# Performance work log

Hardware: AMD Instinct MI355X
Metric: run time of the kernel (lower is better)

The kernel has to match this reference:

```python
import jax, jax.numpy as jnp
import numpy as np

S = 7          # number of slots
B = 8192       # batch
D = 1024       # input_dim
E = 256        # slot_embedding_dim
H = 512        # rnn_hidden_dim
SH = 256       # slot_hidden_dim
V = 100        # labels per slot (uniform)


def _lstm_cell(x, h, c, W_ih, W_hh, b_ih, b_hh):
    # PyTorch LSTMCell: gates ordered i, f, g, o
    gates = x @ W_ih.T + b_ih + h @ W_hh.T + b_hh
    i, f, g, o = jnp.split(gates, 4, axis=-1)
    i = jax.nn.sigmoid(i); f = jax.nn.sigmoid(f)
    g = jnp.tanh(g); o = jax.nn.sigmoid(o)
    c_new = f * c + i * g
    h_new = o * jnp.tanh(c_new)
    return h_new, c_new


def setup_inputs() -> dict:
    key = jax.random.key(0)
    ks = jax.random.split(key, 24)
    sc = 0.05
    D0 = D + E  # layer-0 input size
    inp = {
        'inputs': jax.random.normal(ks[0], (B, D), jnp.float32),
        'labels': jax.random.randint(ks[1], (S - 1, B), 0, V),
        'start': jax.random.normal(ks[2], (E,), jnp.float32),
        'emb': jax.random.normal(ks[3], (S - 1, V, E), jnp.float32) * sc,
        # layer 0 (input size D0)
        'W_ih0': jax.random.normal(ks[4], (S, 4 * H, D0), jnp.float32) * sc,
        'W_hh0': jax.random.normal(ks[5], (S, 4 * H, H), jnp.float32) * sc,
        'b_ih0': jax.random.normal(ks[6], (S, 4 * H), jnp.float32) * sc,
        'b_hh0': jax.random.normal(ks[7], (S, 4 * H), jnp.float32) * sc,
        'hwN_W0': jax.random.normal(ks[8], (S, H, D0 + H), jnp.float32) * sc,
        'hwN_b0': jax.random.normal(ks[9], (S, H), jnp.float32) * sc,
        'hwL_W0': jax.random.normal(ks[10], (S, H, D0), jnp.float32) * sc,
        # layer 1 (input size H)
        'W_ih1': jax.random.normal(ks[11], (S, 4 * H, H), jnp.float32) * sc,
        'W_hh1': jax.random.normal(ks[12], (S, 4 * H, H), jnp.float32) * sc,
        'b_ih1': jax.random.normal(ks[13], (S, 4 * H), jnp.float32) * sc,
        'b_hh1': jax.random.normal(ks[14], (S, 4 * H), jnp.float32) * sc,
        'hwN_W1': jax.random.normal(ks[15], (S, H, H + H), jnp.float32) * sc,
        'hwN_b1': jax.random.normal(ks[16], (S, H), jnp.float32) * sc,
        'hwL_W1': jax.random.normal(ks[17], (S, H, H), jnp.float32) * sc,
        # slot hidden + classifier
        'sh_W': jax.random.normal(ks[18], (S, SH, H), jnp.float32) * sc,
        'sh_b': jax.random.normal(ks[19], (S, SH), jnp.float32) * sc,
        'pred_W': jax.random.normal(ks[20], (S, V, SH), jnp.float32) * sc,
        'pred_b': jax.random.normal(ks[21], (S, V), jnp.float32) * sc,
    }
    return inp


def reference(inputs, labels, start, emb,
              W_ih0, W_hh0, b_ih0, b_hh0, hwN_W0, hwN_b0, hwL_W0,
              W_ih1, W_hh1, b_ih1, b_hh1, hwN_W1, hwN_b1, hwL_W1,
              sh_W, sh_b, pred_W, pred_b):
    bsz = inputs.shape[0]
    cur_emb = jnp.broadcast_to(start[None, :], (bsz, E))
    h0 = jnp.zeros((bsz, H), inputs.dtype); c0 = jnp.zeros((bsz, H), inputs.dtype)
    h1 = jnp.zeros((bsz, H), inputs.dtype); c1 = jnp.zeros((bsz, H), inputs.dtype)
    logits_all = []
    for i in range(S):  # slots are a short, structurally distinct recurrence
        x = jnp.concatenate([inputs, cur_emb], axis=-1)  # [B, D+E]
        # layer 0
        h0, c0 = _lstm_cell(x, h0, c0, W_ih0[i], W_hh0[i], b_ih0[i], b_hh0[i])
        gate = jax.nn.sigmoid(jnp.concatenate([x, h0], -1) @ hwN_W0[i].T + hwN_b0[i])
        cur = gate * h0 + (1.0 - gate) * (x @ hwL_W0[i].T)
        # layer 1
        h1, c1 = _lstm_cell(cur, h1, c1, W_ih1[i], W_hh1[i], b_ih1[i], b_hh1[i])
        gate1 = jax.nn.sigmoid(jnp.concatenate([cur, h1], -1) @ hwN_W1[i].T + hwN_b1[i])
        # (highway output of last layer feeds nothing further for this slot)
        _ = gate1 * h1 + (1.0 - gate1) * (cur @ hwL_W1[i].T)
        hidden = jax.nn.relu(h1 @ sh_W[i].T + sh_b[i])     # [B, SH]
        logits_all.append(hidden @ pred_W[i].T + pred_b[i])  # [B, V]
        if i < S - 1:
            cur_emb = emb[i][labels[i]]  # teacher-forced embedding lookup
    return jnp.stack(logits_all, axis=0)  # [S, B, V]
```

## Files before the change

### kernel.cpp

```cpp
#include <hip/hip_runtime.h>

#define SLOTS 7
#define BATCH 8192

typedef __attribute__((ext_vector_type(8))) __bf16 bf16x8;
typedef __attribute__((ext_vector_type(4))) float f32x4;

__device__ __forceinline__ void gl_lds16(const __bf16* g, __bf16* l) {
  __builtin_amdgcn_global_load_lds(
      (const __attribute__((address_space(1))) void*)g,
      (__attribute__((address_space(3))) void*)l, 16, 0, 0);
}

__device__ __forceinline__ float sigmoidf_(float x) {
  return 1.f / (1.f + __expf(-x));
}
__device__ __forceinline__ float tanhf_(float x) {
  float xc = fminf(fmaxf(x, -15.f), 15.f);
  float e = __expf(2.f * xc);
  return (e - 1.f) / (e + 1.f);
}

__device__ __forceinline__ void xcd_remap(int& bx, int& by) {
  const int NBx = gridDim.x;
  const int NB = NBx * gridDim.y;
  int id = by * NBx + bx;
  id = (id & 7) * (NB >> 3) + (id >> 3);
  bx = id % NBx;
  by = id / NBx;
}

__global__ void __launch_bounds__(256, 4)
gemm_lstm(const __bf16* __restrict__ A, int lda,
          const __bf16* __restrict__ Bw, int ldb,
          const float* __restrict__ b_ih, const float* __restrict__ b_hh,
          float* __restrict__ cst, __bf16* __restrict__ hout, int hld, int hoff,
          int K) {
  __shared__ __align__(16) __bf16 As[2][128 * 32];
  __shared__ __align__(16) __bf16 Bs[2][128 * 32];
  const int w = threadIdx.x >> 6;
  const int lane = threadIdx.x & 63;
  const int wr = w >> 1, wc = w & 1;
  int bx = blockIdx.x, by = blockIdx.y;
  xcd_remap(bx, by);
  const int rowBase = by << 7;
  const int colBase = bx << 7;
  const int sr = lane >> 2;
  const int scs = (((lane & 3) ^ ((sr >> 1) & 3)) << 3);

  f32x4 acc[4][4];
#pragma unroll
  for (int i = 0; i < 4; ++i)
#pragma unroll
    for (int j = 0; j < 4; ++j) acc[i][j] = (f32x4){0.f, 0.f, 0.f, 0.f};

  const int nsteps = K >> 5;

#define STAGE(bi, k0)                                                            \
  {                                                                              \
    const __bf16* ga = A + (size_t)(rowBase + (w << 5) + sr) * lda + (k0) + scs; \
    gl_lds16(ga, &As[(bi)][(w << 5) * 32]);                                      \
    gl_lds16(ga + (size_t)16 * lda, &As[(bi)][((w << 5) + 16) * 32]);            \
    const __bf16* gb = Bw + (size_t)(colBase + (w << 5) + sr) * ldb + (k0) + scs;\
    gl_lds16(gb, &Bs[(bi)][(w << 5) * 32]);                                      \
    gl_lds16(gb + (size_t)16 * ldb, &Bs[(bi)][((w << 5) + 16) * 32]);            \
  }

  STAGE(0, 0);
  __syncthreads();
  int buf = 0;
  const int ln = lane & 15;
  const int lh = lane >> 4;
  const int swz = ((lh ^ ((ln >> 1) & 3)) << 3);
  for (int t = 0; t < nsteps; ++t) {
    if (t + 1 < nsteps) STAGE(buf ^ 1, (t + 1) << 5);
    bf16x8 av[4], bv[4];
#pragma unroll
    for (int i = 0; i < 4; ++i)
      av[i] = *(const bf16x8*)&As[buf][((wr << 6) + (i << 4) + ln) * 32 + swz];
#pragma unroll
    for (int i = 0; i < 4; ++i)
      bv[i] = *(const bf16x8*)&Bs[buf][((wc << 6) + (i << 4) + ln) * 32 + swz];
#pragma unroll
    for (int mi = 0; mi < 4; ++mi)
#pragma unroll
      for (int ni = 0; ni < 4; ++ni)
        acc[mi][ni] = __builtin_amdgcn_mfma_f32_16x16x32_bf16(
            av[mi], bv[ni], acc[mi][ni], 0, 0, 0);
    __syncthreads();
    buf ^= 1;
  }
#undef STAGE

  const int row0 = rowBase + (wr << 6) + (lh << 2);
  const int h = (((colBase >> 6) + wc) << 4) + ln;
  const float bs0 = b_ih[h] + b_hh[h];
  const float bs1 = b_ih[512 + h] + b_hh[512 + h];
  const float bs2 = b_ih[1024 + h] + b_hh[1024 + h];
  const float bs3 = b_ih[1536 + h] + b_hh[1536 + h];
#pragma unroll
  for (int mi = 0; mi < 4; ++mi)
#pragma unroll
    for (int r = 0; r < 4; ++r) {
      const int row = row0 + (mi << 4) + r;
      float gi = sigmoidf_(acc[mi][0][r] + bs0);
      float gf = sigmoidf_(acc[mi][1][r] + bs1);
      float gg = tanhf_(acc[mi][2][r] + bs2);
      float go = sigmoidf_(acc[mi][3][r] + bs3);
      const size_t ci = (size_t)row * 512 + h;
      float cn = gf * cst[ci] + gi * gg;
      cst[ci] = cn;
      hout[(size_t)row * hld + hoff + h] = (__bf16)(go * tanhf_(cn));
    }
}

template <int MODE>
__global__ void __launch_bounds__(256)
gemm_bt(const __bf16* __restrict__ A, int lda,
        const __bf16* __restrict__ Bw, int ldb,
        void* __restrict__ Cout, int ldc,
        const float* __restrict__ bias,
        const __bf16* __restrict__ auxr,
        __bf16* __restrict__ hout, int hld, int hoff,
        const __bf16* __restrict__ hsrc,
        const float* __restrict__ embp, const int* __restrict__ labels, int do_emb,
        int M, int N, int K, int Nreal) {
  __shared__ __align__(16) __bf16 As[2][128 * 32];
  __shared__ __align__(16) __bf16 Bs[2][128 * 32];
  const int w = threadIdx.x >> 6;
  const int lane = threadIdx.x & 63;
  const int wr = w >> 1, wc = w & 1;
  int bx = blockIdx.x, by = blockIdx.y;
  xcd_remap(bx, by);
  const int rowBase = by << 7;
  const int colBase = bx << 7;
  const int sr = lane >> 2;
  const int sc = (lane & 3) << 3;

  f32x4 acc[4][4];
#pragma unroll
  for (int i = 0; i < 4; ++i)
#pragma unroll
    for (int j = 0; j < 4; ++j) acc[i][j] = (f32x4){0.f, 0.f, 0.f, 0.f};

  const int nsteps = K >> 5;

#define STAGE(bi, k0)                                                           \
  {                                                                             \
    const __bf16* ga = A + (size_t)(rowBase + (w << 5) + sr) * lda + (k0) + sc; \
    gl_lds16(ga, &As[(bi)][(w << 5) * 32]);                                     \
    gl_lds16(ga + (size_t)16 * lda, &As[(bi)][((w << 5) + 16) * 32]);           \
    const __bf16* gb = Bw + (size_t)(colBase + (w << 5) + sr) * ldb + (k0) + sc;\
    gl_lds16(gb, &Bs[(bi)][(w << 5) * 32]);                                     \
    gl_lds16(gb + (size_t)16 * ldb, &Bs[(bi)][((w << 5) + 16) * 32]);           \
  }

  STAGE(0, 0);
  __syncthreads();
  int buf = 0;
  const int ln = lane & 15;
  const int kg = (lane >> 4) << 3;
  for (int t = 0; t < nsteps; ++t) {
    if (t + 1 < nsteps) STAGE(buf ^ 1, (t + 1) << 5);
    bf16x8 av[4], bv[4];
#pragma unroll
    for (int i = 0; i < 4; ++i)
      av[i] = *(const bf16x8*)&As[buf][((wr << 6) + (i << 4) + ln) * 32 + kg];
#pragma unroll
    for (int i = 0; i < 4; ++i)
      bv[i] = *(const bf16x8*)&Bs[buf][((wc << 6) + (i << 4) + ln) * 32 + kg];
#pragma unroll
    for (int mi = 0; mi < 4; ++mi)
#pragma unroll
      for (int ni = 0; ni < 4; ++ni)
        acc[mi][ni] = __builtin_amdgcn_mfma_f32_16x16x32_bf16(
            av[mi], bv[ni], acc[mi][ni], 0, 0, 0);
    __syncthreads();
    buf ^= 1;
  }
#undef STAGE

  const int lh = lane >> 4;
  const int row0 = rowBase + (wr << 6) + (lh << 2);
  const int col0 = colBase + (wc << 6) + ln;

  if (MODE == 1) {
    __bf16* C = (__bf16*)Cout;
#pragma unroll
    for (int mi = 0; mi < 4; ++mi)
#pragma unroll
      for (int ni = 0; ni < 4; ++ni) {
        const int col = col0 + (ni << 4);
        const float b = bias[col];
#pragma unroll
        for (int r = 0; r < 4; ++r) {
          float v = fmaxf(acc[mi][ni][r] + b, 0.f);
          C[(size_t)(row0 + (mi << 4) + r) * ldc + col] = (__bf16)v;
        }
      }
  } else if (MODE == 2) {
    float* C = (float*)Cout;
#pragma unroll
    for (int mi = 0; mi < 4; ++mi)
#pragma unroll
      for (int ni = 0; ni < 4; ++ni) {
        const int col = col0 + (ni << 4);
        if (col < Nreal) {
          const float b = bias[col];
#pragma unroll
          for (int r = 0; r < 4; ++r)
            C[(size_t)(row0 + (mi << 4) + r) * ldc + col] = acc[mi][ni][r] + b;
        }
      }
  } else if (MODE == 7) {
    __bf16* C = (__bf16*)Cout;
#pragma unroll
    for (int mi = 0; mi < 4; ++mi)
#pragma unroll
      for (int ni = 0; ni < 4; ++ni) {
        const int col = col0 + (ni << 4);
#pragma unroll
        for (int r = 0; r < 4; ++r)
          C[(size_t)(row0 + (mi << 4) + r) * ldc + col] = (__bf16)acc[mi][ni][r];
      }
  } else if (MODE == 6) {
    __bf16* C = (__bf16*)Cout;
#pragma unroll
    for (int mi = 0; mi < 4; ++mi)
#pragma unroll
      for (int ni = 0; ni < 4; ++ni) {
        const int col = col0 + (ni << 4);
#pragma unroll
        for (int r = 0; r < 4; ++r) {
          const int row = row0 + (mi << 4) + r;
          float xp = (float)auxr[(size_t)row * 1024 + col];
          float hwl = (float)auxr[(size_t)row * 1024 + 512 + col];
          float gn = sigmoidf_(acc[mi][ni][r] + xp + bias[col]);
          float hn = (float)hsrc[(size_t)row * 512 + col];
          C[(size_t)row * ldc + col] = (__bf16)(gn * hn + (1.f - gn) * hwl);
          hout[(size_t)row * hld + hoff + col] = (__bf16)hn;
        }
      }
    if (do_emb && colBase < 256) {
#pragma unroll
      for (int mi = 0; mi < 4; ++mi)
#pragma unroll
        for (int r = 0; r < 4; ++r) {
          const int row = row0 + (mi << 4) + r;
          const int lab = labels[row];
#pragma unroll
          for (int ni = 0; ni < 4; ++ni) {
            const int col = col0 + (ni << 4);
            hout[(size_t)row * hld + 1024 + col] =
                (__bf16)embp[(size_t)lab * 256 + col];
          }
        }
    }
  }
}

#define PR0 2621440
#define PR1 3670016
#define PR2 4325376
#define PR3 4980736
#define PR4 5242880
#define PR5 6291456
#define PR6 7340032
#define PR7 7471104
#define PR8 7503872
__global__ void pack_all(const float* __restrict__ W_ih0, const float* __restrict__ W_hh0,
                         const float* __restrict__ hwN_W0, const float* __restrict__ hwL_W0,
                         const float* __restrict__ W_ih1, const float* __restrict__ W_hh1,
                         const float* __restrict__ sh_W, const float* __restrict__ pred_W,
                         __bf16* __restrict__ WA, __bf16* __restrict__ WX,
                         __bf16* __restrict__ WH, __bf16* __restrict__ WB,
                         __bf16* __restrict__ WS, __bf16* __restrict__ WP, int s) {
  const int idx = blockIdx.x * 256 + threadIdx.x;
  if (idx >= PR8) return;
  if (idx < PR0) {
    int i = idx, r = i / 1280, c = i - r * 1280;
    int sr = (((r >> 4) & 3) << 9) + ((r >> 6) << 4) + (r & 15);
    WA[(long)r * 1792 + c] = (__bf16)W_ih0[(size_t)s * 2048 * 1280 + (long)sr * 1280 + c];
  } else if (idx < PR1) {
    int i = idx - PR0, r = i >> 9, c = i & 511;
    int sr = (((r >> 4) & 3) << 9) + ((r >> 6) << 4) + (r & 15);
    WA[(long)r * 1792 + 1280 + c] = (__bf16)W_hh0[(size_t)s * 2048 * 512 + (long)sr * 512 + c];
  } else if (idx < PR2) {
    int i = idx - PR1, r = i / 1280, c = i - r * 1280;
    WX[(long)r * 1280 + c] = (__bf16)hwN_W0[(size_t)s * 512 * 1792 + (long)r * 1792 + c];
  } else if (idx < PR3) {
    int i = idx - PR2, r = i / 1280, c = i - r * 1280;
    WX[(long)(512 + r) * 1280 + c] = (__bf16)hwL_W0[(size_t)s * 512 * 1280 + (long)r * 1280 + c];
  } else if (idx < PR4) {
    int i = idx - PR3, r = i >> 9, c = i & 511;
    WH[(long)r * 512 + c] = (__bf16)hwN_W0[(size_t)s * 512 * 1792 + (long)r * 1792 + 1280 + c];
  } else if (idx < PR5) {
    int i = idx - PR4, r = i >> 9, c = i & 511;
    int sr = (((r >> 4) & 3) << 9) + ((r >> 6) << 4) + (r & 15);
    WB[(long)r * 1024 + c] = (__bf16)W_ih1[(size_t)s * 2048 * 512 + (long)sr * 512 + c];
  } else if (idx < PR6) {
    int i = idx - PR5, r = i >> 9, c = i & 511;
    int sr = (((r >> 4) & 3) << 9) + ((r >> 6) << 4) + (r & 15);
    WB[(long)r * 1024 + 512 + c] = (__bf16)W_hh1[(size_t)s * 2048 * 512 + (long)sr * 512 + c];
  } else if (idx < PR7) {
    int i = idx - PR6, r = i >> 9, c = i & 511;
    WS[(long)r * 512 + c] = (__bf16)sh_W[(size_t)s * 256 * 512 + (long)r * 512 + c];
  } else {
    int i = idx - PR7, r = i >> 8, c = i & 255;
    float v = (r < 100) ? pred_W[(size_t)s * 100 * 256 + (long)r * 256 + c] : 0.f;
    WP[(long)r * 256 + c] = (__bf16)v;
  }
}

__global__ void conv_inputs(const float* __restrict__ in, __bf16* __restrict__ xh) {
  int idx = blockIdx.x * 256 + threadIdx.x;
  int b = idx >> 10, c = idx & 1023;
  xh[(size_t)b * 1792 + c] = (__bf16)in[idx];
}

__global__ void set_start(const float* __restrict__ start, __bf16* __restrict__ xh) {
  int idx = blockIdx.x * 256 + threadIdx.x;
  int b = idx >> 8, e = idx & 255;
  xh[(size_t)b * 1792 + 1024 + e] = (__bf16)start[e];
}

__global__ void zero_states(__bf16* __restrict__ xh, __bf16* __restrict__ xh1A) {
  int idx = blockIdx.x * 256 + threadIdx.x;
  int b = idx >> 9, h = idx & 511;
  xh[(size_t)b * 1792 + 1280 + h] = (__bf16)0.f;
  xh1A[(size_t)b * 1024 + 512 + h] = (__bf16)0.f;
}

extern "C" void kernel_launch(void* const* d_in, const int* in_sizes, int n_in,
                              void* d_out, int out_size, void* d_ws, size_t ws_size,
                              hipStream_t stream) {
  const float* inputs = (const float*)d_in[0];
  const int* labels = (const int*)d_in[1];
  const float* start = (const float*)d_in[2];
  const float* emb = (const float*)d_in[3];
  const float* W_ih0 = (const float*)d_in[4];
  const float* W_hh0 = (const float*)d_in[5];
  const float* b_ih0 = (const float*)d_in[6];
  const float* b_hh0 = (const float*)d_in[7];
  const float* hwN_W0 = (const float*)d_in[8];
  const float* hwN_b0 = (const float*)d_in[9];
  const float* hwL_W0 = (const float*)d_in[10];
  const float* W_ih1 = (const float*)d_in[11];
  const float* W_hh1 = (const float*)d_in[12];
  const float* b_ih1 = (const float*)d_in[13];
  const float* b_hh1 = (const float*)d_in[14];
  const float* sh_W = (const float*)d_in[18];
  const float* sh_b = (const float*)d_in[19];
  const float* pred_W = (const float*)d_in[20];
  const float* pred_b = (const float*)d_in[21];
  float* out = (float*)d_out;

  char* p = (char*)d_ws;
  size_t off = 0;
  auto alloc = [&](size_t bytes) {
    void* r = p + off;
    off += (bytes + 255) & ~(size_t)255;
    return r;
  };
  __bf16* WA = (__bf16*)alloc((size_t)2048 * 1792 * 2);
  __bf16* WX = (__bf16*)alloc((size_t)1024 * 1280 * 2);
  __bf16* WH = (__bf16*)alloc((size_t)512 * 512 * 2);
  __bf16* WB = (__bf16*)alloc((size_t)2048 * 1024 * 2);
  __bf16* WS = (__bf16*)alloc((size_t)256 * 512 * 2);
  __bf16* WP = (__bf16*)alloc((size_t)128 * 256 * 2);
  __bf16* xh = (__bf16*)alloc((size_t)BATCH * 1792 * 2);
  __bf16* xh1A = (__bf16*)alloc((size_t)BATCH * 1024 * 2);
  __bf16* xh1B = (__bf16*)alloc((size_t)BATCH * 1024 * 2);
  __bf16* h0new = (__bf16*)alloc((size_t)BATCH * 512 * 2);
  __bf16* ghw = (__bf16*)alloc((size_t)BATCH * 1024 * 2);
  float* c0 = (float*)alloc((size_t)BATCH * 512 * 4);
  float* c1 = (float*)alloc((size_t)BATCH * 512 * 4);
  __bf16* hidden = (__bf16*)ghw;
  (void)ws_size; (void)in_sizes; (void)n_in; (void)out_size;

  hipMemsetAsync(c0, 0, (size_t)BATCH * 512 * 4, stream);
  hipMemsetAsync(c1, 0, (size_t)BATCH * 512 * 4, stream);
  zero_states<<<BATCH * 512 / 256, 256, 0, stream>>>(xh, xh1A);
  conv_inputs<<<BATCH * 1024 / 256, 256, 0, stream>>>(inputs, xh);
  set_start<<<BATCH * 256 / 256, 256, 0, stream>>>(start, xh);

  const dim3 blk(256);
  for (int s = 0; s < SLOTS; ++s) {
    __bf16* xcur = (s & 1) ? xh1B : xh1A;
    __bf16* xnext = (s & 1) ? xh1A : xh1B;
    pack_all<<<(PR8 + 255) / 256, blk, 0, stream>>>(
        W_ih0, W_hh0, hwN_W0, hwL_W0, W_ih1, W_hh1, sh_W, pred_W,
        WA, WX, WH, WB, WS, WP, s);

    gemm_bt<7><<<dim3(8, 64), blk, 0, stream>>>(
        xh, 1792, WX, 1280, ghw, 1024, nullptr,
        nullptr, nullptr, 0, 0, nullptr, nullptr, nullptr, 0,
        BATCH, 1024, 1280, 1024);
    gemm_lstm<<<dim3(16, 64), blk, 0, stream>>>(
        xh, 1792, WA, 1792, b_ih0 + s * 2048, b_hh0 + s * 2048,
        c0, h0new, 512, 0, 1792);
    gemm_bt<6><<<dim3(4, 64), blk, 0, stream>>>(
        h0new, 512, WH, 512, xcur, 1024, hwN_b0 + s * 512,
        ghw, xh, 1792, 1280, h0new,
        emb + (size_t)s * 100 * 256, labels + (size_t)s * BATCH,
        (s < SLOTS - 1) ? 1 : 0, BATCH, 512, 512, 512);
    gemm_lstm<<<dim3(16, 64), blk, 0, stream>>>(
        xcur, 1024, WB, 1024, b_ih1 + s * 2048, b_hh1 + s * 2048,
        c1, xnext, 1024, 512, 1024);
    gemm_bt<1><<<dim3(2, 64), blk, 0, stream>>>(
        xnext + 512, 1024, WS, 512, hidden, 256, sh_b + s * 256,
        nullptr, nullptr, 0, 0, nullptr, nullptr, nullptr, 0,
        BATCH, 256, 512, 256);
    gemm_bt<2><<<dim3(1, 64), blk, 0, stream>>>(
        hidden, 256, WP, 256, out + (size_t)s * BATCH * 100, 100,
        pred_b + s * 100, nullptr, nullptr, 0, 0, nullptr, nullptr, nullptr, 0,
        BATCH, 128, 256, 100);
  }
}
```

Before: 1.584 ms.

## Fuse layer-0 GEMMs, swizzle LDS, and fuse slot-hidden and classifier head

The layer-0 gate GEMM and the highway-input projection GEMM now run as one launch: block columns 0-15 compute the LSTM gates and the remaining 8 compute the projection. That launch also adds an XOR swizzle of LDS chunk placement to cut bank conflicts on the fragment reads. The slot-hidden ReLU GEMM and the classifier GEMM are merged into one 512-thread kernel that keeps the hidden tile in LDS, so it is never written to and re-read from global memory, and one launch per slot is dropped. The risk is that the fused head runs only 64 large blocks using about 114 KB of LDS each, which leaves most CUs idle for that stage. The classifier also reads its weights directly from global memory.

```diff
diff --git a/kernel.cpp b/kernel.cpp
--- a/kernel.cpp
+++ b/kernel.cpp
@@ -28,6 +28,106 @@
   id = (id & 7) * (NB >> 3) + (id >> 3);
   bx = id % NBx;
   by = id / NBx;
+}
+
+__global__ void __launch_bounds__(256, 4)
+gemm0_fused(const __bf16* __restrict__ A, int lda,
+            const __bf16* __restrict__ WA, const __bf16* __restrict__ WX,
+            const float* __restrict__ b_ih, const float* __restrict__ b_hh,
+            float* __restrict__ cst, __bf16* __restrict__ hout, int hld, int hoff,
+            __bf16* __restrict__ ghw) {
+  __shared__ __align__(16) __bf16 As[2][128 * 32];
+  __shared__ __align__(16) __bf16 Bs[2][128 * 32];
+  const int w = threadIdx.x >> 6;
+  const int lane = threadIdx.x & 63;
+  const int wr = w >> 1, wc = w & 1;
+  int bx = blockIdx.x, by = blockIdx.y;
+  xcd_remap(bx, by);
+  const bool isAux = (bx >= 16);
+  const int rowBase = by << 7;
+  const int colBase = (isAux ? (bx - 16) : bx) << 7;
+  const __bf16* Bw = isAux ? WX : WA;
+  const int ldb = isAux ? 1280 : 1792;
+  const int nsteps = (isAux ? 1280 : 1792) >> 5;
+  const int sr = lane >> 2;
+  const int scs = (((lane & 3) ^ ((sr >> 1) & 3)) << 3);
+
+  f32x4 acc[4][4];
+#pragma unroll
+  for (int i = 0; i < 4; ++i)
+#pragma unroll
+    for (int j = 0; j < 4; ++j) acc[i][j] = (f32x4){0.f, 0.f, 0.f, 0.f};
+
+#define STAGE(bi, k0)                                                            \
+  {                                                                              \
+    const __bf16* ga = A + (size_t)(rowBase + (w << 5) + sr) * lda + (k0) + scs; \
+    gl_lds16(ga, &As[(bi)][(w << 5) * 32]);                                      \
+    gl_lds16(ga + (size_t)16 * lda, &As[(bi)][((w << 5) + 16) * 32]);            \
+    const __bf16* gb = Bw + (size_t)(colBase + (w << 5) + sr) * ldb + (k0) + scs;\
+    gl_lds16(gb, &Bs[(bi)][(w << 5) * 32]);                                      \
+    gl_lds16(gb + (size_t)16 * ldb, &Bs[(bi)][((w << 5) + 16) * 32]);            \
+  }
+
+  STAGE(0, 0);
+  __syncthreads();
+  int buf = 0;
+  const int ln = lane & 15;
+  const int lh = lane >> 4;
+  const int swz = ((lh ^ ((ln >> 1) & 3)) << 3);
+  for (int t = 0; t < nsteps; ++t) {
+    if (t + 1 < nsteps) STAGE(buf ^ 1, (t + 1) << 5);
+    bf16x8 av[4], bv[4];
+#pragma unroll
+    for (int i = 0; i < 4; ++i)
+      av[i] = *(const bf16x8*)&As[buf][((wr << 6) + (i << 4) + ln) * 32 + swz];
+#pragma unroll
+    for (int i = 0; i < 4; ++i)
+      bv[i] = *(const bf16x8*)&Bs[buf][((wc << 6) + (i << 4) + ln) * 32 + swz];
+#pragma unroll
+    for (int mi = 0; mi < 4; ++mi)
+#pragma unroll
+      for (int ni = 0; ni < 4; ++ni)
+        acc[mi][ni] = __builtin_amdgcn_mfma_f32_16x16x32_bf16(
+            av[mi], bv[ni], acc[mi][ni], 0, 0, 0);
+    __syncthreads();
+    buf ^= 1;
+  }
+#undef STAGE
+
+  const int row0 = rowBase + (wr << 6) + (lh << 2);
+  if (!isAux) {
+    const int h = (((colBase >> 6) + wc) << 4) + ln;
+    const float bs0 = b_ih[h] + b_hh[h];
+    const float bs1 = b_ih[512 + h] + b_hh[512 + h];
+    const float bs2 = b_ih[1024 + h] + b_hh[1024 + h];
+    const float bs3 = b_ih[1536 + h] + b_hh[1536 + h];
+#pragma unroll
+    for (int mi = 0; mi < 4; ++mi)
+#pragma unroll
+      for (int r = 0; r < 4; ++r) {
+        const int row = row0 + (mi << 4) + r;
+        float gi = sigmoidf_(acc[mi][0][r] + bs0);
+        float gf = sigmoidf_(acc[mi][1][r] + bs1);
+        float gg = tanhf_(acc[mi][2][r] + bs2);
+        float go = sigmoidf_(acc[mi][3][r] + bs3);
+        const size_t ci = (size_t)row * 512 + h;
+        float cn = gf * cst[ci] + gi * gg;
+        cst[ci] = cn;
+        hout[(size_t)row * hld + hoff + h] = (__bf16)(go * tanhf_(cn));
+      }
+  } else {
+    const int col0 = colBase + (wc << 6) + ln;
+#pragma unroll
+    for (int mi = 0; mi < 4; ++mi)
+#pragma unroll
+      for (int ni = 0; ni < 4; ++ni) {
+        const int col = col0 + (ni << 4);
+#pragma unroll
+        for (int r = 0; r < 4; ++r)
+          ghw[(size_t)(row0 + (mi << 4) + r) * 1024 + col] =
+              (__bf16)acc[mi][ni][r];
+      }
+  }
 }
 
 __global__ void __launch_bounds__(256, 4)
@@ -114,17 +214,16 @@
     }
 }
 
-template <int MODE>
 __global__ void __launch_bounds__(256)
-gemm_bt(const __bf16* __restrict__ A, int lda,
-        const __bf16* __restrict__ Bw, int ldb,
-        void* __restrict__ Cout, int ldc,
-        const float* __restrict__ bias,
-        const __bf16* __restrict__ auxr,
-        __bf16* __restrict__ hout, int hld, int hoff,
-        const __bf16* __restrict__ hsrc,
-        const float* __restrict__ embp, const int* __restrict__ labels, int do_emb,
-        int M, int N, int K, int Nreal) {
+gemm_hwy(const __bf16* __restrict__ A, int lda,
+         const __bf16* __restrict__ Bw, int ldb,
+         __bf16* __restrict__ Cout, int ldc,
+         const float* __restrict__ bias,
+         const __bf16* __restrict__ auxr,
+         __bf16* __restrict__ hout, int hld, int hoff,
+         const __bf16* __restrict__ hsrc,
+         const float* __restrict__ embp, const int* __restrict__ labels,
+         int do_emb) {
   __shared__ __align__(16) __bf16 As[2][128 * 32];
   __shared__ __align__(16) __bf16 Bs[2][128 * 32];
   const int w = threadIdx.x >> 6;
@@ -143,7 +242,7 @@
 #pragma unroll
     for (int j = 0; j < 4; ++j) acc[i][j] = (f32x4){0.f, 0.f, 0.f, 0.f};
 
-  const int nsteps = K >> 5;
+  const int nsteps = 512 >> 5;
 
 #define STAGE(bi, k0)                                                           \
   {                                                                             \
@@ -183,79 +282,151 @@
   const int lh = lane >> 4;
   const int row0 = rowBase + (wr << 6) + (lh << 2);
   const int col0 = colBase + (wc << 6) + ln;
-
-  if (MODE == 1) {
-    __bf16* C = (__bf16*)Cout;
+#pragma unroll
+  for (int mi = 0; mi < 4; ++mi)
+#pragma unroll
+    for (int ni = 0; ni < 4; ++ni) {
+      const int col = col0 + (ni << 4);
+#pragma unroll
+      for (int r = 0; r < 4; ++r) {
+        const int row = row0 + (mi << 4) + r;
+        float xp = (float)auxr[(size_t)row * 1024 + col];
+        float hwl = (float)auxr[(size_t)row * 1024 + 512 + col];
+        float gn = sigmoidf_(acc[mi][ni][r] + xp + bias[col]);
+        float hn = (float)hsrc[(size_t)row * 512 + col];
+        Cout[(size_t)row * ldc + col] = (__bf16)(gn * hn + (1.f - gn) * hwl);
+        hout[(size_t)row * hld + hoff + col] = (__bf16)hn;
+      }
+    }
+  if (do_emb && colBase < 256) {
+#pragma unroll
+    for (int mi = 0; mi < 4; ++mi)
+#pragma unroll
+      for (int r = 0; r < 4; ++r) {
+        const int row = row0 + (mi << 4) + r;
+        const int lab = labels[row];
+#pragma unroll
+        for (int ni = 0; ni < 4; ++ni) {
+          const int col = col0 + (ni << 4);
+          hout[(size_t)row * hld + 1024 + col] =
+              (__bf16)embp[(size_t)lab * 256 + col];
+        }
+      }
+  }
+}
+
+__global__ void __launch_bounds__(512)
+head_fused(const __bf16* __restrict__ h1, int lda,
+           const __bf16* __restrict__ WS, const float* __restrict__ sh_b,
+           const __bf16* __restrict__ WP, const float* __restrict__ pred_b,
+           float* __restrict__ out) {
+  extern __shared__ __bf16 dls[];
+  __bf16* As = dls;
+  __bf16* Bs = dls + 8192;
+  __bf16* hid = dls + 24576;
+  const int w = threadIdx.x >> 6;
+  const int lane = threadIdx.x & 63;
+  const int wr = w >> 2, wc = w & 3;
+  const int rowBase = blockIdx.x << 7;
+  const int sr = lane >> 2;
+  const int sc = (lane & 3) << 3;
+  const int ln = lane & 15;
+  const int lh = lane >> 4;
+  const int kg = lh << 3;
+
+  f32x4 acc[4][4];
+#pragma unroll
+  for (int i = 0; i < 4; ++i)
+#pragma unroll
+    for (int j = 0; j < 4; ++j) acc[i][j] = (f32x4){0.f, 0.f, 0.f, 0.f};
+
+#define STAGEH(bi, k0)                                                          \
+  {                                                                             \
+    const __bf16* ga = h1 + (size_t)(rowBase + (w << 4) + sr) * lda + (k0) + sc;\
+    gl_lds16(ga, As + (bi)*4096 + (w << 4) * 32);                               \
+    const __bf16* gb = WS + (size_t)((w << 5) + sr) * 512 + (k0) + sc;          \
+    gl_lds16(gb, Bs + (bi)*8192 + (w << 5) * 32);                               \
+    gl_lds16(gb + (size_t)16 * 512, Bs + (bi)*8192 + ((w << 5) + 16) * 32);     \
+  }
+
+  STAGEH(0, 0);
+  __syncthreads();
+  int buf = 0;
+  for (int t = 0; t < 16; ++t) {
+    if (t + 1 < 16) STAGEH(buf ^ 1, (t + 1) << 5);
+    bf16x8 av[4], bv[4];
+#pragma unroll
+    for (int i = 0; i < 4; ++i)
+      av[i] = *(const bf16x8*)&As[buf * 4096 + ((wr << 6) + (i << 4) + ln) * 32 + kg];
+#pragma unroll
+    for (int i = 0; i < 4; ++i)
+      bv[i] = *(const bf16x8*)&Bs[buf * 8192 + ((wc << 6) + (i << 4) + ln) * 32 + kg];
+#pragma unroll
+    for (int mi = 0; mi < 4; ++mi)
+#pragma unroll
+      for (int ni = 0; ni < 4; ++ni)
+        acc[mi][ni] = __builtin_amdgcn_mfma_f32_16x16x32_bf16(
+            av[mi], bv[ni], acc[mi][ni], 0, 0, 0);
+    __syncthreads();
+    buf ^= 1;
+  }
+#undef STAGEH
+
+  {
+    const int rl0 = (wr << 6) + (lh << 2);
+    const int cl0 = (wc << 6) + ln;
+#pragma unroll
+    for (int mi = 0; mi < 4; ++mi)
+#pragma unroll
+      for (int ni = 0; ni < 4; ++ni) {
+        const int col = cl0 + (ni << 4);
+        const float b = sh_b[col];
+#pragma unroll
+        for (int r = 0; r < 4; ++r) {
+          float v = fmaxf(acc[mi][ni][r] + b, 0.f);
+          hid[(rl0 + (mi << 4) + r) * 264 + col] = (__bf16)v;
+        }
+      }
+  }
+  __syncthreads();
+
+  if (w < 4) {
+    const int wr2 = w >> 1, wc2 = w & 1;
+    f32x4 a2[4][4];
+#pragma unroll
+    for (int i = 0; i < 4; ++i)
+#pragma unroll
+      for (int j = 0; j < 4; ++j) a2[i][j] = (f32x4){0.f, 0.f, 0.f, 0.f};
+    for (int t = 0; t < 8; ++t) {
+      bf16x8 av[4], bv[4];
+#pragma unroll
+      for (int i = 0; i < 4; ++i)
+        av[i] = *(const bf16x8*)&hid[((wr2 << 6) + (i << 4) + ln) * 264 + (t << 5) + kg];
+#pragma unroll
+      for (int i = 0; i < 4; ++i)
+        bv[i] = *(const bf16x8*)&WP[(size_t)((wc2 << 6) + (i << 4) + ln) * 256 + (t << 5) + kg];
+#pragma unroll
+      for (int mi = 0; mi < 4; ++mi)
+#pragma unroll
+        for (int ni = 0; ni < 4; ++ni)
+          a2[mi][ni] = __builtin_amdgcn_mfma_f32_16x16x32_bf16(
+              av[mi], bv[ni], a2[mi][ni], 0, 0, 0);
+    }
+    const int row0 = rowBase + (wr2 << 6) + (lh << 2);
+    const int col0 = (wc2 << 6) + ln;
 #pragma unroll
     for (int mi = 0; mi < 4; ++mi)
 #pragma unroll
       for (int ni = 0; ni < 4; ++ni) {
         const int col = col0 + (ni << 4);
-        const float b = bias[col];
-#pragma unroll
-        for (int r = 0; r < 4; ++r) {
-          float v = fmaxf(acc[mi][ni][r] + b, 0.f);
-          C[(size_t)(row0 + (mi << 4) + r) * ldc + col] = (__bf16)v;
+        if (col < 100) {
+          const float b = pred_b[col];
+#pragma unroll
+          for (int r = 0; r < 4; ++r)
+            out[(size_t)(row0 + (mi << 4) + r) * 100 + col] =
+                a2[mi][ni][r] + b;
         }
       }
-  } else if (MODE == 2) {
-    float* C = (float*)Cout;
-#pragma unroll
-    for (int mi = 0; mi < 4; ++mi)
-#pragma unroll
-      for (int ni = 0; ni < 4; ++ni) {
-        const int col = col0 + (ni << 4);
-        if (col < Nreal) {
-          const float b = bias[col];
-#pragma unroll
-          for (int r = 0; r < 4; ++r)
-            C[(size_t)(row0 + (mi << 4) + r) * ldc + col] = acc[mi][ni][r] + b;
-        }
-      }
-  } else if (MODE == 7) {
-    __bf16* C = (__bf16*)Cout;
-#pragma unroll
-    for (int mi = 0; mi < 4; ++mi)
-#pragma unroll
-      for (int ni = 0; ni < 4; ++ni) {
-        const int col = col0 + (ni << 4);
-#pragma unroll
-        for (int r = 0; r < 4; ++r)
-          C[(size_t)(row0 + (mi << 4) + r) * ldc + col] = (__bf16)acc[mi][ni][r];
-      }
-  } else if (MODE == 6) {
-    __bf16* C = (__bf16*)Cout;
-#pragma unroll
-    for (int mi = 0; mi < 4; ++mi)
-#pragma unroll
-      for (int ni = 0; ni < 4; ++ni) {
-        const int col = col0 + (ni << 4);
-#pragma unroll
-        for (int r = 0; r < 4; ++r) {
-          const int row = row0 + (mi << 4) + r;
-          float xp = (float)auxr[(size_t)row * 1024 + col];
-          float hwl = (float)auxr[(size_t)row * 1024 + 512 + col];
-          float gn = sigmoidf_(acc[mi][ni][r] + xp + bias[col]);
-          float hn = (float)hsrc[(size_t)row * 512 + col];
-          C[(size_t)row * ldc + col] = (__bf16)(gn * hn + (1.f - gn) * hwl);
-          hout[(size_t)row * hld + hoff + col] = (__bf16)hn;
-        }
-      }
-    if (do_emb && colBase < 256) {
-#pragma unroll
-      for (int mi = 0; mi < 4; ++mi)
-#pragma unroll
-        for (int r = 0; r < 4; ++r) {
-          const int row = row0 + (mi << 4) + r;
-          const int lab = labels[row];
-#pragma unroll
-          for (int ni = 0; ni < 4; ++ni) {
-            const int col = col0 + (ni << 4);
-            hout[(size_t)row * hld + 1024 + col] =
-                (__bf16)embp[(size_t)lab * 256 + col];
-          }
-        }
-    }
   }
 }
 
@@ -375,7 +546,6 @@
   __bf16* ghw = (__bf16*)alloc((size_t)BATCH * 1024 * 2);
   float* c0 = (float*)alloc((size_t)BATCH * 512 * 4);
   float* c1 = (float*)alloc((size_t)BATCH * 512 * 4);
-  __bf16* hidden = (__bf16*)ghw;
   (void)ws_size; (void)in_sizes; (void)n_in; (void)out_size;
 
   hipMemsetAsync(c0, 0, (size_t)BATCH * 512 * 4, stream);
@@ -392,28 +562,19 @@
         W_ih0, W_hh0, hwN_W0, hwL_W0, W_ih1, W_hh1, sh_W, pred_W,
         WA, WX, WH, WB, WS, WP, s);
 
-    gemm_bt<7><<<dim3(8, 64), blk, 0, stream>>>(
-        xh, 1792, WX, 1280, ghw, 1024, nullptr,
-        nullptr, nullptr, 0, 0, nullptr, nullptr, nullptr, 0,
-        BATCH, 1024, 1280, 1024);
-    gemm_lstm<<<dim3(16, 64), blk, 0, stream>>>(
-        xh, 1792, WA, 1792, b_ih0 + s * 2048, b_hh0 + s * 2048,
-        c0, h0new, 512, 0, 1792);
-    gemm_bt<6><<<dim3(4, 64), blk, 0, stream>>>(
+    gemm0_fused<<<dim3(24, 64), blk, 0, stream>>>(
+        xh, 1792, WA, WX, b_ih0 + s * 2048, b_hh0 + s * 2048,
+        c0, h0new, 512, 0, ghw);
+    gemm_hwy<<<dim3(4, 64), blk, 0, stream>>>(
         h0new, 512, WH, 512, xcur, 1024, hwN_b0 + s * 512,
         ghw, xh, 1792, 1280, h0new,
         emb + (size_t)s * 100 * 256, labels + (size_t)s * BATCH,
-        (s < SLOTS - 1) ? 1 : 0, BATCH, 512, 512, 512);
+        (s < SLOTS - 1) ? 1 : 0);
     gemm_lstm<<<dim3(16, 64), blk, 0, stream>>>(
         xcur, 1024, WB, 1024, b_ih1 + s * 2048, b_hh1 + s * 2048,
         c1, xnext, 1024, 512, 1024);
-    gemm_bt<1><<<dim3(2, 64), blk, 0, stream>>>(
-        xnext + 512, 1024, WS, 512, hidden, 256, sh_b + s * 256,
-        nullptr, nullptr, 0, 0, nullptr, nullptr, nullptr, 0,
-        BATCH, 256, 512, 256);
-    gemm_bt<2><<<dim3(1, 64), blk, 0, stream>>>(
-        hidden, 256, WP, 256, out + (size_t)s * BATCH * 100, 100,
-        pred_b + s * 100, nullptr, nullptr, 0, 0, nullptr, nullptr, nullptr, 0,
-        BATCH, 128, 256, 100);
-  }
-}
+    head_fused<<<64, 512, 116736, stream>>>(
+        xnext + 512, 1024, WS, sh_b + s * 256, WP, pred_b + s * 100,
+        out + (size_t)s * BATCH * 100);
+  }
+}
```

Measured after the change: 1.597 ms. About the same (+0.8%).
